# Performance work log

Measured on AMD Instinct MI355X. Metric: run time of the kernel, lower is better.

The kernel has to match this reference:

```python
import jax, jax.numpy as jnp
import numpy as np

B, S, D, H = 2, 2048, 1024, 16
DK = D // H

def setup_inputs() -> dict:
    key = jax.random.key(0)
    ks = jax.random.split(key, 12)
    s = 1.0 / np.sqrt(D)
    inp = {
        'q': jax.random.normal(ks[0], (B, S, D), jnp.float32),
        'k': jax.random.normal(ks[1], (B, S, D), jnp.float32),
        'v': jax.random.normal(ks[2], (B, S, D), jnp.float32),
        'mask': jnp.tril(jnp.ones((S, S), jnp.int32))[None, None],  # [1,1,S,S] causal
        'Wq': jax.random.normal(ks[3], (D, D), jnp.float32) * s,
        'bq': jax.random.normal(ks[4], (D,), jnp.float32) * s,
        'Wk': jax.random.normal(ks[5], (D, D), jnp.float32) * s,
        'bk': jax.random.normal(ks[6], (D,), jnp.float32) * s,
        'Wv': jax.random.normal(ks[7], (D, D), jnp.float32) * s,
        'bv': jax.random.normal(ks[8], (D,), jnp.float32) * s,
        'Wo': jax.random.normal(ks[9], (D, D), jnp.float32) * s,
        'bo': jax.random.normal(ks[10], (D,), jnp.float32) * s,
    }
    return inp

def reference(q, k, v, mask, Wq, bq, Wk, bk, Wv, bv, Wo, bo):
    # linear projections (torch nn.Linear: x @ W.T + b)
    query = q @ Wq.T + bq
    key_ = k @ Wk.T + bk
    value = v @ Wv.T + bv
    # [B,S,D] -> [B,H,S,dk]
    def split_heads(x):
        return x.reshape(B, S, H, DK).transpose(0, 2, 1, 3)
    query, key_, value = split_heads(query), split_heads(key_), split_heads(value)
    scores = jnp.einsum('bhqd,bhkd->bhqk', query, key_) / jnp.sqrt(jnp.float32(DK))
    scores = jnp.where(mask == 0, jnp.float32(-1e9), scores)
    # FAITHFUL to source: softmax over dim=1 (the HEAD axis), not dim=-1
    attn = jax.nn.softmax(scores, axis=1)
    x = jnp.einsum('bhqk,bhkd->bhqd', attn, value)
    x = x.transpose(0, 2, 1, 3).reshape(B, S, D)
    return x @ Wo.T + bo
```

## Files before the change

### kernel.cpp

```cpp
#include <hip/hip_runtime.h>
#include <hip/hip_bf16.h>
#include <stdint.h>
#include <stddef.h>


typedef __attribute__((ext_vector_type(8))) __bf16 bf16x8;
typedef __attribute__((ext_vector_type(4))) __bf16 bf16x4;
typedef __attribute__((ext_vector_type(4))) _Float16 f16x4;
typedef __attribute__((ext_vector_type(8))) _Float16 f16x8;
typedef __attribute__((ext_vector_type(4))) float  f32x4;
typedef __attribute__((ext_vector_type(8))) float  f32x8;

#define MFMA_BF16_K32(a,b,c) __builtin_amdgcn_mfma_f32_16x16x32_bf16((a),(b),(c),0,0,0)
#define MFMA_F16_K16(a,b,c)  __builtin_amdgcn_mfma_f32_16x16x16f16((a),(b),(c),0,0,0)

template <typename T> __device__ inline f32x8 ld8(const T* p);
template <> __device__ inline f32x8 ld8<float>(const float* p) { return *(const f32x8*)p; }
template <> __device__ inline f32x8 ld8<__bf16>(const __bf16* p) {
  return __builtin_convertvector(*(const bf16x8*)p, f32x8);
}

__device__ __forceinline__ void gl_lds16(const __bf16* g, __bf16* l) {
  __builtin_amdgcn_global_load_lds(
      (const __attribute__((address_space(1))) void*)g,
      (__attribute__((address_space(3))) void*)l, 16, 0, 0);
}

__device__ __forceinline__ void epi_store(int mode, float val, int m, int n, void* dst) {
  if (mode == 0) {
    ((float*)dst)[(size_t)m * 1024 + n] = val;
  } else if (mode == 2) {
    const int bb = m >> 11, s = m & 2047, h = n >> 6, dhi = (n >> 5) & 1, dlo = n & 31;
    ((__bf16*)dst)[(size_t)((h * 2 + dhi) * 2 + bb) * 65536 + s * 32 + dlo] = (__bf16)val;
  } else {
    const int bb = m >> 11, s = m & 2047, h = n >> 6, d = n & 63;
    ((_Float16*)dst)[((((size_t)bb * 128 + (s >> 4)) * 16 + h) * 64 + d) * 16 + (s & 15)] =
        (_Float16)val;
  }
}

struct CvtArgs { const float* src[7]; __bf16* dst[7]; };

__global__ __launch_bounds__(256) void cvt_kernel(CvtArgs a, int nqkv, int nw) {
  const int t = blockIdx.y;
  const int n = (t < 3) ? nqkv : nw;
  const int base = (blockIdx.x * 256 + threadIdx.x) * 8;
  if (base >= n) return;
  *(bf16x8*)(a.dst[t] + base) =
      __builtin_convertvector(*(const f32x8*)(a.src[t] + base), bf16x8);
}

struct GemmSet {
  const __bf16* A0[3]; const __bf16* A1[3]; const __bf16* A2[3]; const __bf16* A3[3];
  const __bf16* W[3]; const float* bias[3]; void* dst[3]; int mode[3];
};

__global__ __launch_bounds__(256) void gemm_tile(GemmSet g) {
  const int z = blockIdx.z;
  const __bf16* __restrict__ A0 = g.A0[z];
  const __bf16* __restrict__ A1 = g.A1[z];
  const __bf16* __restrict__ A2 = g.A2[z];
  const __bf16* __restrict__ A3 = g.A3[z];
  const __bf16* __restrict__ W  = g.W[z];
  const float*  __restrict__ bias = g.bias[z];
  void* dst = g.dst[z];
  const int mode = g.mode[z];

  __shared__ __bf16 As[128 * 64];
  __shared__ __bf16 Bs[128 * 64];
  const int tid  = threadIdx.x;
  const int lane = tid & 63, wid = tid >> 6;
  const int l15  = lane & 15, quad = lane >> 4;
  const int m0   = blockIdx.y * 128;
  const int n0   = blockIdx.x * 128;
  const int srow = lane >> 3;
  const int swz  = ((lane & 7) ^ srow) * 8;
  const int wm   = (wid >> 1) * 64;
  const int wn   = (wid & 1) * 64;
  const int mr = tid >> 3;
  const int mc = tid & 7;
  const int mg = ((mc ^ (mr & 7)) * 8);

  f32x4 acc[4][4] = {};

  for (int k0 = 0; k0 < 1024; k0 += 64) {
    if (A1 != nullptr) {
      #pragma unroll
      for (int gI = 0; gI < 4; ++gI) {
        const size_t gi = (size_t)(m0 + gI * 32 + mr) * 1024 + k0 + mg;
        f32x8 s = ld8(&A0[gi]) + ld8(&A1[gi]) + ld8(&A2[gi]) + ld8(&A3[gi]);
        *(bf16x8*)&As[(gI * 32 + mr) * 64 + mc * 8] = __builtin_convertvector(s, bf16x8);
      }
    } else {
      #pragma unroll
      for (int i = 0; i < 4; ++i)
        gl_lds16(A0 + (size_t)(m0 + wid * 32 + i * 8 + srow) * 1024 + k0 + swz,
                 &As[(wid * 32 + i * 8) * 64]);
    }
    #pragma unroll
    for (int i = 0; i < 4; ++i)
      gl_lds16(W + (size_t)(n0 + wid * 32 + i * 8 + srow) * 1024 + k0 + swz,
               &Bs[(wid * 32 + i * 8) * 64]);
    __syncthreads();
    #pragma unroll
    for (int kk = 0; kk < 64; kk += 32) {
      const int slot = (((kk >> 3) + quad) ^ (l15 & 7)) * 8;
      bf16x8 fa[4], fb[4];
      #pragma unroll
      for (int ms = 0; ms < 4; ++ms)
        fa[ms] = *(const bf16x8*)&As[(wm + ms * 16 + l15) * 64 + slot];
      #pragma unroll
      for (int ns = 0; ns < 4; ++ns)
        fb[ns] = *(const bf16x8*)&Bs[(wn + ns * 16 + l15) * 64 + slot];
      #pragma unroll
      for (int ms = 0; ms < 4; ++ms)
        #pragma unroll
        for (int ns = 0; ns < 4; ++ns)
          acc[ms][ns] = MFMA_BF16_K32(fa[ms], fb[ns], acc[ms][ns]);
    }
    __syncthreads();
  }

  #pragma unroll
  for (int ms = 0; ms < 4; ++ms) {
    #pragma unroll
    for (int ns = 0; ns < 4; ++ns) {
      const int n     = n0 + wn + ns * 16 + l15;
      const float bv  = bias[n];
      const int mbase = m0 + wm + ms * 16 + quad * 4;
      #pragma unroll
      for (int r = 0; r < 4; ++r)
        epi_store(mode, acc[ms][ns][r] + bv, mbase + r, n, dst);
    }
  }
}

template <typename TA>
__global__ __launch_bounds__(256) void gemm_bt(
    const TA* __restrict__ A0, const TA* __restrict__ A1,
    const float* __restrict__ W, const float* __restrict__ bias,
    void* dst, int mode)
{
  __shared__ __bf16 As[64][72];
  __shared__ __bf16 Bs[64][72];
  const int tid  = threadIdx.x;
  const int m0   = blockIdx.y * 64;
  const int n0   = blockIdx.x * 64;
  const int row  = tid >> 3;
  const int seg  = (tid & 7) * 8;
  const int lane = tid & 63;
  const int wid  = tid >> 6;
  const int l15  = lane & 15;
  const int quad = lane >> 4;
  const int wm   = (wid >> 1) * 32;
  const int wn   = (wid & 1) * 32;

  f32x4 acc[2][2] = {};

  for (int k0 = 0; k0 < 1024; k0 += 64) {
    const size_t i0 = (size_t)(m0 + row) * 1024 + k0 + seg;
    const size_t i1 = (size_t)(m0 + row + 32) * 1024 + k0 + seg;
    f32x8 a0 = ld8(&A0[i0]);
    f32x8 a1 = ld8(&A0[i1]);
    if (A1) { a0 += ld8(&A1[i0]); a1 += ld8(&A1[i1]); }
    f32x8 b0 = ld8(&W[(size_t)(n0 + row) * 1024 + k0 + seg]);
    f32x8 b1 = ld8(&W[(size_t)(n0 + row + 32) * 1024 + k0 + seg]);
    *(bf16x8*)&As[row][seg]      = __builtin_convertvector(a0, bf16x8);
    *(bf16x8*)&As[row + 32][seg] = __builtin_convertvector(a1, bf16x8);
    *(bf16x8*)&Bs[row][seg]      = __builtin_convertvector(b0, bf16x8);
    *(bf16x8*)&Bs[row + 32][seg] = __builtin_convertvector(b1, bf16x8);
    __syncthreads();
    #pragma unroll
    for (int kk = 0; kk < 64; kk += 32) {
      bf16x8 fa0 = *(const bf16x8*)&As[wm + l15][kk + quad * 8];
      bf16x8 fa1 = *(const bf16x8*)&As[wm + 16 + l15][kk + quad * 8];
      bf16x8 fb0 = *(const bf16x8*)&Bs[wn + l15][kk + quad * 8];
      bf16x8 fb1 = *(const bf16x8*)&Bs[wn + 16 + l15][kk + quad * 8];
      acc[0][0] = MFMA_BF16_K32(fa0, fb0, acc[0][0]);
      acc[0][1] = MFMA_BF16_K32(fa0, fb1, acc[0][1]);
      acc[1][0] = MFMA_BF16_K32(fa1, fb0, acc[1][0]);
      acc[1][1] = MFMA_BF16_K32(fa1, fb1, acc[1][1]);
    }
    __syncthreads();
  }

  #pragma unroll
  for (int ms = 0; ms < 2; ++ms) {
    #pragma unroll
    for (int ns = 0; ns < 2; ++ns) {
      const int n     = n0 + wn + ns * 16 + l15;
      const float bv  = bias[n];
      const int mbase = m0 + wm + ms * 16 + quad * 4;
      #pragma unroll
      for (int r = 0; r < 4; ++r)
        epi_store(mode, acc[ms][ns][r] + bv, mbase + r, n, dst);
    }
  }
}

__global__ __launch_bounds__(256) void sufscan_kernel(
    const _Float16* __restrict__ Vl, float* __restrict__ suffix)
{
  const int gid = blockIdx.x * 256 + threadIdx.x;
  const int hd = gid & 1023;
  const int b  = gid >> 10;
  float run = 0.f;
  for (int kt = 127; kt >= 0; --kt) {
    suffix[((size_t)(b * 128 + kt)) * 1024 + hd] = run * 0.0625f;
    const _Float16* p = Vl + ((size_t)(b * 128 + kt) * 1024 + hd) * 16;
    f32x8 s = __builtin_convertvector(*(const f16x8*)p, f32x8) +
              __builtin_convertvector(*(const f16x8*)(p + 8), f32x8);
    float tot = 0.f;
    #pragma unroll
    for (int i = 0; i < 8; ++i) tot += s[i];
    run += tot;
  }
}

__global__ __launch_bounds__(256, 2) void attn_kernel(
    const __bf16* __restrict__ Qs, const __bf16* __restrict__ Ks,
    const _Float16* __restrict__ Vl, const float* __restrict__ suffix,
    __bf16* __restrict__ P0, __bf16* __restrict__ P1,
    __bf16* __restrict__ P2, __bf16* __restrict__ P3, int lnsl)
{
  __shared__ float Pf[2][2][4][16][20];

  const int tid   = threadIdx.x;
  const int nsl   = 1 << lnsl;
  const int slice = blockIdx.x & (nsl - 1);
  const int rest  = blockIdx.x >> lnsl;
  const int b     = rest & 1;
  const int t     = 127 - (rest >> 1);
  const int q0    = t * 16;
  const int nt    = t + 1;
  const int tbeg  = (slice * nt) >> lnsl;
  const int tend  = ((slice + 1) * nt) >> lnsl;

  const int lane = tid & 63, wid = tid >> 6;
  const int l15 = lane & 15, quad = lane >> 4;
  const float kSc = 0.18033688011112042f;

  bf16x8 qf[4][2];
  #pragma unroll
  for (int hh = 0; hh < 4; ++hh) {
    const int h = wid * 4 + hh;
    #pragma unroll
    for (int dhi = 0; dhi < 2; ++dhi)
      qf[hh][dhi] = *(const bf16x8*)&Qs[(size_t)((h * 2 + dhi) * 2 + b) * 65536
                                        + (q0 + l15) * 32 + quad * 8];
  }

  f32x4 acc[4][4] = {};
  int buf = 0;

  for (int ct = tbeg; ct < tend; ct += 2, buf ^= 1) {
    const int ntc = (tend - ct) < 2 ? 1 : 2;
    const int cc1 = (ct + 1 < 128) ? ct + 1 : 127;
    const int ccl[2] = {ct, cc1};

    bf16x8 kf[4][2][2];
    #pragma unroll
    for (int hh = 0; hh < 4; ++hh) {
      const int h = wid * 4 + hh;
      #pragma unroll
      for (int j = 0; j < 2; ++j) {
        const int krow = ccl[j] * 16 + l15;
        #pragma unroll
        for (int dhi = 0; dhi < 2; ++dhi)
          kf[hh][j][dhi] = *(const bf16x8*)&Ks[(size_t)((h * 2 + dhi) * 2 + b) * 65536
                                                + krow * 32 + quad * 8];
      }
    }

    float e[4][2][4];
    float ps[2][4] = {};
    #pragma unroll
    for (int hh = 0; hh < 4; ++hh) {
      #pragma unroll
      for (int j = 0; j < 2; ++j) {
        f32x4 s = {};
        s = MFMA_BF16_K32(kf[hh][j][0], qf[hh][0], s);
        s = MFMA_BF16_K32(kf[hh][j][1], qf[hh][1], s);
        #pragma unroll
        for (int r = 0; r < 4; ++r) {
          const bool masked = ((ct + j) * 16 + quad * 4 + r) > (q0 + l15);
          const float x = masked ? 0.f : s[r] * kSc;
          float ev = exp2f(x);
          if (j >= ntc) ev = 0.f;
          e[hh][j][r] = ev;
          ps[j][r] += ev;
        }
      }
    }
    #pragma unroll
    for (int j = 0; j < 2; ++j) {
      f32x4 v; v[0] = ps[j][0]; v[1] = ps[j][1]; v[2] = ps[j][2]; v[3] = ps[j][3];
      *(f32x4*)&Pf[buf][j][wid][l15][quad * 4] = v;
    }

    f16x4 vf[4][2][4];
    #pragma unroll
    for (int hh = 0; hh < 4; ++hh) {
      const int h = wid * 4 + hh;
      #pragma unroll
      for (int j = 0; j < 2; ++j) {
        const _Float16* vb = Vl + ((size_t)(b * 128 + ccl[j]) * 16 + h) * 1024;
        #pragma unroll
        for (int n = 0; n < 4; ++n)
          vf[hh][j][n] = *(const f16x4*)(vb + (n * 16 + l15) * 16 + quad * 4);
      }
    }
    __syncthreads();

    float inv[2][4];
    #pragma unroll
    for (int j = 0; j < 2; ++j) {
      f32x4 tot = *(const f32x4*)&Pf[buf][j][0][l15][quad * 4];
      #pragma unroll
      for (int w = 1; w < 4; ++w)
        tot += *(const f32x4*)&Pf[buf][j][w][l15][quad * 4];
      #pragma unroll
      for (int r = 0; r < 4; ++r) inv[j][r] = 1.f / fmaxf(tot[r], 1e-30f);
    }

    #pragma unroll
    for (int hh = 0; hh < 4; ++hh) {
      #pragma unroll
      for (int j = 0; j < 2; ++j) {
        if (j >= ntc) break;
        f16x4 af;
        #pragma unroll
        for (int r = 0; r < 4; ++r) af[r] = (_Float16)(e[hh][j][r] * inv[j][r]);
        #pragma unroll
        for (int n = 0; n < 4; ++n)
          acc[hh][n] = MFMA_F16_K16(af, vf[hh][j][n], acc[hh][n]);
      }
    }
  }

  __bf16* Pout = slice == 0 ? P0 : slice == 1 ? P1 : slice == 2 ? P2 : P3;
  const bool last = (slice == nsl - 1);
  #pragma unroll
  for (int hh = 0; hh < 4; ++hh) {
    const int h = wid * 4 + hh;
    #pragma unroll
    for (int n = 0; n < 4; ++n) {
      const float sfx =
          last ? suffix[((size_t)(b * 128 + t)) * 1024 + h * 64 + n * 16 + l15] : 0.f;
      #pragma unroll
      for (int r = 0; r < 4; ++r)
        Pout[((size_t)(b * 2048 + q0 + quad * 4 + r)) * 1024 + h * 64 + n * 16 + l15] =
            (__bf16)(acc[hh][n][r] + sfx);
    }
  }
}

extern "C" void kernel_launch(void* const* d_in, const int* in_sizes, int n_in,
                              void* d_out, int out_size, void* d_ws, size_t ws_size,
                              hipStream_t stream) {
  const float* q  = (const float*)d_in[0];
  const float* k  = (const float*)d_in[1];
  const float* v  = (const float*)d_in[2];
  const float* Wq = (const float*)d_in[4];
  const float* bq = (const float*)d_in[5];
  const float* Wk = (const float*)d_in[6];
  const float* bk = (const float*)d_in[7];
  const float* Wv = (const float*)d_in[8];
  const float* bv = (const float*)d_in[9];
  const float* Wo = (const float*)d_in[10];
  const float* bo = (const float*)d_in[11];

  char* ws = (char*)d_ws;
  const size_t MiB = 1ull << 20;

  if (ws_size >= 67 * MiB) {
    __bf16* qc  = (__bf16*)(ws +  0 * MiB);
    __bf16* kc  = (__bf16*)(ws +  8 * MiB);
    __bf16* vc  = (__bf16*)(ws + 16 * MiB);
    __bf16* Wqc = (__bf16*)(ws + 24 * MiB);
    __bf16* Wkc = (__bf16*)(ws + 26 * MiB);
    __bf16* Wvc = (__bf16*)(ws + 28 * MiB);
    __bf16* Woc = (__bf16*)(ws + 30 * MiB);
    __bf16* Qs  = (__bf16*)(ws + 32 * MiB);
    __bf16* Ks  = (__bf16*)(ws + 40 * MiB);
    _Float16* Vl = (_Float16*)(ws + 48 * MiB);
    __bf16* P0  = (__bf16*)(ws + 56 * MiB);
    float* suffix = (float*)(ws + 64 * MiB);

    CvtArgs ca;
    ca.src[0] = q;  ca.dst[0] = qc;
    ca.src[1] = k;  ca.dst[1] = kc;
    ca.src[2] = v;  ca.dst[2] = vc;
    ca.src[3] = Wq; ca.dst[3] = Wqc;
    ca.src[4] = Wk; ca.dst[4] = Wkc;
    ca.src[5] = Wv; ca.dst[5] = Wvc;
    ca.src[6] = Wo; ca.dst[6] = Woc;
    cvt_kernel<<<dim3(2048, 7), 256, 0, stream>>>(ca, 4194304, 1048576);

    GemmSet g3 = {};
    g3.A0[0] = qc; g3.W[0] = Wqc; g3.bias[0] = bq; g3.dst[0] = Qs; g3.mode[0] = 2;
    g3.A0[1] = kc; g3.W[1] = Wkc; g3.bias[1] = bk; g3.dst[1] = Ks; g3.mode[1] = 2;
    g3.A0[2] = vc; g3.W[2] = Wvc; g3.bias[2] = bv; g3.dst[2] = Vl; g3.mode[2] = 3;
    gemm_tile<<<dim3(8, 32, 3), 256, 0, stream>>>(g3);

    sufscan_kernel<<<8, 256, 0, stream>>>(Vl, suffix);
    attn_kernel<<<1024, 256, 0, stream>>>(Qs, Ks, Vl, suffix, P0, qc, kc, vc, 2);

    GemmSet go = {};
    go.A0[0] = P0; go.A1[0] = qc; go.A2[0] = kc; go.A3[0] = vc;
    go.W[0] = Woc; go.bias[0] = bo; go.dst[0] = d_out; go.mode[0] = 0;
    gemm_tile<<<dim3(8, 32, 1), 256, 0, stream>>>(go);
  } else {
    __bf16* Qs  = (__bf16*)(ws);
    __bf16* Ks  = (__bf16*)(ws +  8 * MiB);
    _Float16* Vl = (_Float16*)(ws + 16 * MiB);
    __bf16* P0  = (__bf16*)(ws + 24 * MiB);
    __bf16* P1  = (__bf16*)(ws + 32 * MiB);
    float* suffix = (float*)(ws + 40 * MiB);

    dim3 gg(16, 64, 1);
    gemm_bt<float><<<gg, 256, 0, stream>>>(q, nullptr, Wq, bq, Qs, 2);
    gemm_bt<float><<<gg, 256, 0, stream>>>(k, nullptr, Wk, bk, Ks, 2);
    gemm_bt<float><<<gg, 256, 0, stream>>>(v, nullptr, Wv, bv, Vl, 3);
    sufscan_kernel<<<8, 256, 0, stream>>>(Vl, suffix);
    attn_kernel<<<512, 256, 0, stream>>>(Qs, Ks, Vl, suffix, P0, P1, P1, P1, 1);
    gemm_bt<__bf16><<<gg, 256, 0, stream>>>(P0, P1, Wo, bo, d_out, 0);
  }
}
```

Measured before the change: 354.7 us.

## Parallelize suffix scan, prefetch K tiles, simplify causal mask in attention

The serial suffix-scan kernel (8 blocks, each thread walking 128 tiles and reading 32 bytes per step) is split into a fully parallel tile-sum kernel and a lightweight scan over the precomputed sums. The attention loop now loads the next pair of K tiles before the barrier so global latency overlaps compute, and applies the causal mask only on the diagonal tile. It also uses the hardware reciprocal and packed fp16 conversion for the probabilities. These trade one extra launch and workspace buffer, plus extra registers for the prefetched K, for better parallelism and overlap.

After: 357.3 us. No clear change (+0.7%).

```diff
diff --git a/kernel.cpp b/kernel.cpp
--- a/kernel.cpp
+++ b/kernel.cpp
@@ -6,6 +6,7 @@
 
 typedef __attribute__((ext_vector_type(8))) __bf16 bf16x8;
 typedef __attribute__((ext_vector_type(4))) __bf16 bf16x4;
+typedef __attribute__((ext_vector_type(2))) _Float16 f16x2;
 typedef __attribute__((ext_vector_type(4))) _Float16 f16x4;
 typedef __attribute__((ext_vector_type(8))) _Float16 f16x8;
 typedef __attribute__((ext_vector_type(4))) float  f32x4;
@@ -24,6 +25,10 @@
   __builtin_amdgcn_global_load_lds(
       (const __attribute__((address_space(1))) void*)g,
       (__attribute__((address_space(3))) void*)l, 16, 0, 0);
+}
+
+__device__ __forceinline__ f16x2 pk2(float a, float b) {
+  return __builtin_bit_cast(f16x2, __builtin_amdgcn_cvt_pkrtz(a, b));
 }
 
 __device__ __forceinline__ void epi_store(int mode, float val, int m, int n, void* dst) {
@@ -198,6 +203,35 @@
   }
 }
 
+__global__ __launch_bounds__(256) void tilesum_kernel(
+    const _Float16* __restrict__ Vl, float* __restrict__ tsum)
+{
+  const int gid = blockIdx.x * 256 + threadIdx.x;
+  const _Float16* p = Vl + (size_t)gid * 16;
+  f32x8 s = __builtin_convertvector(*(const f16x8*)p, f32x8) +
+            __builtin_convertvector(*(const f16x8*)(p + 8), f32x8);
+  float tot = 0.f;
+  #pragma unroll
+  for (int i = 0; i < 8; ++i) tot += s[i];
+  tsum[gid] = tot;
+}
+
+__global__ __launch_bounds__(64) void scan_kernel(
+    const float* __restrict__ tsum, float* __restrict__ suffix)
+{
+  const int gid = blockIdx.x * 64 + threadIdx.x;
+  const int hd = gid & 1023;
+  const int b  = gid >> 10;
+  const float* tp = tsum + (size_t)b * 131072 + hd;
+  float* sp = suffix + (size_t)b * 131072 + hd;
+  float run = 0.f;
+  #pragma unroll 4
+  for (int kt = 127; kt >= 0; --kt) {
+    sp[(size_t)kt * 1024] = run * 0.0625f;
+    run += tp[(size_t)kt * 1024];
+  }
+}
+
 __global__ __launch_bounds__(256) void sufscan_kernel(
     const _Float16* __restrict__ Vl, float* __restrict__ suffix)
 {
@@ -253,12 +287,10 @@
   f32x4 acc[4][4] = {};
   int buf = 0;
 
-  for (int ct = tbeg; ct < tend; ct += 2, buf ^= 1) {
-    const int ntc = (tend - ct) < 2 ? 1 : 2;
+  bf16x8 kf[4][2][2];
+  auto load_k = [&](int ct) {
     const int cc1 = (ct + 1 < 128) ? ct + 1 : 127;
     const int ccl[2] = {ct, cc1};
-
-    bf16x8 kf[4][2][2];
     #pragma unroll
     for (int hh = 0; hh < 4; ++hh) {
       const int h = wid * 4 + hh;
@@ -271,6 +303,13 @@
                                                 + krow * 32 + quad * 8];
       }
     }
+  };
+  if (tbeg < tend) load_k(tbeg);
+
+  for (int ct = tbeg; ct < tend; ct += 2, buf ^= 1) {
+    const int ntc = (tend - ct) < 2 ? 1 : 2;
+    const int cc1 = (ct + 1 < 128) ? ct + 1 : 127;
+    const int ccl[2] = {ct, cc1};
 
     float e[4][2][4];
     float ps[2][4] = {};
@@ -281,10 +320,11 @@
         f32x4 s = {};
         s = MFMA_BF16_K32(kf[hh][j][0], qf[hh][0], s);
         s = MFMA_BF16_K32(kf[hh][j][1], qf[hh][1], s);
+        const bool dg = (ccl[j] == t);
         #pragma unroll
         for (int r = 0; r < 4; ++r) {
-          const bool masked = ((ct + j) * 16 + quad * 4 + r) > (q0 + l15);
-          const float x = masked ? 0.f : s[r] * kSc;
+          float x = s[r] * kSc;
+          if (dg) x = (quad * 4 + r > l15) ? 0.f : x;
           float ev = exp2f(x);
           if (j >= ntc) ev = 0.f;
           e[hh][j][r] = ev;
@@ -310,6 +350,9 @@
           vf[hh][j][n] = *(const f16x4*)(vb + (n * 16 + l15) * 16 + quad * 4);
       }
     }
+
+    if (ct + 2 < tend) load_k(ct + 2);
+
     __syncthreads();
 
     float inv[2][4];
@@ -320,7 +363,8 @@
       for (int w = 1; w < 4; ++w)
         tot += *(const f32x4*)&Pf[buf][j][w][l15][quad * 4];
       #pragma unroll
-      for (int r = 0; r < 4; ++r) inv[j][r] = 1.f / fmaxf(tot[r], 1e-30f);
+      for (int r = 0; r < 4; ++r)
+        inv[j][r] = __builtin_amdgcn_rcpf(fmaxf(tot[r], 1e-30f));
     }
 
     #pragma unroll
@@ -328,9 +372,9 @@
       #pragma unroll
       for (int j = 0; j < 2; ++j) {
         if (j >= ntc) break;
-        f16x4 af;
-        #pragma unroll
-        for (int r = 0; r < 4; ++r) af[r] = (_Float16)(e[hh][j][r] * inv[j][r]);
+        f16x2 lo = pk2(e[hh][j][0] * inv[j][0], e[hh][j][1] * inv[j][1]);
+        f16x2 hi = pk2(e[hh][j][2] * inv[j][2], e[hh][j][3] * inv[j][3]);
+        f16x4 af = __builtin_shufflevector(lo, hi, 0, 1, 2, 3);
         #pragma unroll
         for (int n = 0; n < 4; ++n)
           acc[hh][n] = MFMA_F16_K16(af, vf[hh][j][n], acc[hh][n]);
@@ -386,6 +430,7 @@
     _Float16* Vl = (_Float16*)(ws + 48 * MiB);
     __bf16* P0  = (__bf16*)(ws + 56 * MiB);
     float* suffix = (float*)(ws + 64 * MiB);
+    float* tsum   = (float*)(ws + 65 * MiB);
 
     CvtArgs ca;
     ca.src[0] = q;  ca.dst[0] = qc;
@@ -403,7 +448,8 @@
     g3.A0[2] = vc; g3.W[2] = Wvc; g3.bias[2] = bv; g3.dst[2] = Vl; g3.mode[2] = 3;
     gemm_tile<<<dim3(8, 32, 3), 256, 0, stream>>>(g3);
 
-    sufscan_kernel<<<8, 256, 0, stream>>>(Vl, suffix);
+    tilesum_kernel<<<1024, 256, 0, stream>>>(Vl, tsum);
+    scan_kernel<<<32, 64, 0, stream>>>(tsum, suffix);
     attn_kernel<<<1024, 256, 0, stream>>>(Qs, Ks, Vl, suffix, P0, qc, kc, vc, 2);
 
     GemmSet go = {};
```
